# Kernel tuning notes

Measured on AMD Instinct MI355X. Metric: run time of the kernel, lower is better.

## Reference

```python
import jax, jax.numpy as jnp
import numpy as np


def setup_inputs() -> dict:
    key = jax.random.key(0)
    k1, k2 = jax.random.split(key)
    vortex_feature = jax.random.normal(k1, (2, 512, 6), dtype=jnp.float32)
    points = jax.random.normal(k2, (2, 256, 256, 2), dtype=jnp.float32)
    return {"vortex_feature": vortex_feature, "points": points}


def reference(vortex_feature, points):
    # vortex_feature: [B, N, 6] -> (y, x, tau, sig, v, u)
    y, x, tau, sig, v, u = [vortex_feature[..., i] for i in range(6)]
    loc = jnp.stack([y, x], axis=-1)            # [B, N, 2]

    # Broadcast: points [B, H, W, 1, 2] vs particle locations [B, 1, 1, N, 2]
    distances = points[..., None, :] - loc[:, None, None, :, :]   # [B, H, W, N, 2]
    sq_distance = jnp.sum(distances ** 2, axis=-1, keepdims=True)  # [B, H, W, N, 1]

    src_sigma = sig[:, None, None, :, None]     # [B, 1, 1, N, 1]
    src_strength = tau[:, None, None, :, None]  # [B, 1, 1, N, 1]

    falloff = jnp.exp(-sq_distance / src_sigma ** 2) / jnp.sqrt(sq_distance)
    strength = src_strength * falloff           # [B, H, W, N, 1]

    d1 = distances[..., 0]
    d2 = distances[..., 1]
    velocity = strength * jnp.stack([d2, -d1], axis=-1)  # [B, H, W, N, 2]
    return jnp.sum(velocity, axis=-2)           # [B, H, W, 2]
```

## Files before the change

### kernel.cpp

```cpp
#include <hip/hip_runtime.h>

#ifndef M_LOG2E_F
#define M_LOG2E_F 1.4426950408889634f
#endif

#if defined(__has_builtin)
#  if __has_builtin(__builtin_amdgcn_exp2f)
#    define FAST_EXP2(x) __builtin_amdgcn_exp2f(x)
#  else
#    define FAST_EXP2(x) exp2f(x)
#  endif
#  if __has_builtin(__builtin_amdgcn_rsqf)
#    define FAST_RSQ(x) __builtin_amdgcn_rsqf(x)
#  else
#    define FAST_RSQ(x) rsqrtf(x)
#  endif
#else
#  define FAST_EXP2(x) exp2f(x)
#  define FAST_RSQ(x) rsqrtf(x)
#endif

__global__ __launch_bounds__(256)
void GaussianFalloffKernel_83434034692733_kernel(
    const float* __restrict__ vortex,
    const float* __restrict__ points,
    float* __restrict__ out)
{
    constexpr int NV = 512;
    constexpr int PTS_PER_BATCH = 256 * 256;
    constexpr int BLOCKS_PER_BATCH = PTS_PER_BATCH / 256;

    __shared__ float4 sv[NV];

    const int b  = blockIdx.x / BLOCKS_PER_BATCH;
    const int pt = (blockIdx.x % BLOCKS_PER_BATCH) * 256 + threadIdx.x;

    const float* __restrict__ vb = vortex + (size_t)b * NV * 6;
    for (int v = threadIdx.x; v < NV; v += 256) {
        const float y   = vb[v * 6 + 0];
        const float x   = vb[v * 6 + 1];
        const float tau = vb[v * 6 + 2];
        const float sig = vb[v * 6 + 3];
        const float k   = M_LOG2E_F / (sig * sig);
        sv[v] = make_float4(y, x, tau, k);
    }
    __syncthreads();

    const float2 p = ((const float2*)points)[(size_t)b * PTS_PER_BATCH + pt];

    float acc0 = 0.0f;
    float acc1 = 0.0f;

    #pragma unroll 8
    for (int v = 0; v < NV; ++v) {
        const float4 s = sv[v];
        const float dy = p.x - s.x;
        const float dx = p.y - s.y;
        const float r2 = fmaf(dy, dy, dx * dx);
        const float e  = FAST_EXP2(-r2 * s.w);
        const float ri = FAST_RSQ(r2);
        const float f  = s.z * e * ri;
        acc0 = fmaf(f,  dx, acc0);
        acc1 = fmaf(f, -dy, acc1);
    }

    ((float2*)out)[(size_t)b * PTS_PER_BATCH + pt] = make_float2(acc0, acc1);
}

extern "C" void kernel_launch(void* const* d_in, const int* in_sizes, int n_in,
                              void* d_out, int out_size, void* d_ws, size_t ws_size,
                              hipStream_t stream) {
    const float* vortex = (const float*)d_in[0];
    const float* points = (const float*)d_in[1];
    float* out = (float*)d_out;

    const int blocks = 2 * 256;
    GaussianFalloffKernel_83434034692733_kernel<<<blocks, 256, 0, stream>>>(
        vortex, points, out);
}
```

Before: 80.51 us.

## Split vortex loop across four wavefronts, two points per thread with packed math

Each block now handles 128 points instead of 256. Its four wavefronts each sum a quarter of the vortices, and the partial sums are combined through shared memory. Each thread processes two points with 2-wide vector types so the compiler can emit packed FP32 ops, and each shared-memory vortex load now serves two points. The grid doubles to 1024 blocks to fill the CUs better. In exchange it adds a reduction step, an extra barrier and more shared memory.

Result: faster. 73.32 us (-8.9%).

```diff
diff --git a/kernel.cpp b/kernel.cpp
--- a/kernel.cpp
+++ b/kernel.cpp
@@ -1,8 +1,6 @@
 #include <hip/hip_runtime.h>
 
-#ifndef M_LOG2E_F
-#define M_LOG2E_F 1.4426950408889634f
-#endif
+typedef float v2f __attribute__((ext_vector_type(2)));
 
 #if defined(__has_builtin)
 #  if __has_builtin(__builtin_amdgcn_exp2f)
@@ -20,51 +18,73 @@
 #  define FAST_RSQ(x) rsqrtf(x)
 #endif
 
-__global__ __launch_bounds__(256)
+__global__ __launch_bounds__(256, 4)
 void GaussianFalloffKernel_83434034692733_kernel(
     const float* __restrict__ vortex,
     const float* __restrict__ points,
     float* __restrict__ out)
 {
     constexpr int NV = 512;
-    constexpr int PTS_PER_BATCH = 256 * 256;
-    constexpr int BLOCKS_PER_BATCH = PTS_PER_BATCH / 256;
+    constexpr int NQ = 4;
+    constexpr int VQ = NV / NQ;
+    constexpr int PTS_PER_BLOCK = 128;
+    constexpr int BLOCKS_PER_BATCH = 65536 / PTS_PER_BLOCK;
 
     __shared__ float4 sv[NV];
+    __shared__ v2f    red[NQ][PTS_PER_BLOCK];
 
-    const int b  = blockIdx.x / BLOCKS_PER_BATCH;
-    const int pt = (blockIdx.x % BLOCKS_PER_BATCH) * 256 + threadIdx.x;
+    const int b    = blockIdx.x / BLOCKS_PER_BATCH;
+    const int base = (blockIdx.x % BLOCKS_PER_BATCH) * PTS_PER_BLOCK;
+
+    const int tid = threadIdx.x;
+    const int q   = tid >> 6;
+    const int h   = tid & 63;
 
     const float* __restrict__ vb = vortex + (size_t)b * NV * 6;
-    for (int v = threadIdx.x; v < NV; v += 256) {
-        const float y   = vb[v * 6 + 0];
-        const float x   = vb[v * 6 + 1];
-        const float tau = vb[v * 6 + 2];
-        const float sig = vb[v * 6 + 3];
-        const float k   = M_LOG2E_F / (sig * sig);
-        sv[v] = make_float4(y, x, tau, k);
+    for (int v = tid; v < NV; v += 256) {
+        const float y    = vb[v * 6 + 0];
+        const float x    = vb[v * 6 + 1];
+        const float tau  = vb[v * 6 + 2];
+        const float sig  = vb[v * 6 + 3];
+        const float negk = -1.4426950408889634f / (sig * sig);
+        sv[v] = make_float4(y, x, tau, negk);
     }
     __syncthreads();
 
-    const float2 p = ((const float2*)points)[(size_t)b * PTS_PER_BATCH + pt];
+    const float2* __restrict__ pp =
+        (const float2*)points + (size_t)b * 65536 + base;
+    const float2 pA = pp[h];
+    const float2 pB = pp[h + 64];
+    const v2f py = { pA.x, pB.x };
+    const v2f px = { pA.y, pB.y };
 
-    float acc0 = 0.0f;
-    float acc1 = 0.0f;
+    v2f acc0 = { 0.0f, 0.0f };
+    v2f acc1 = { 0.0f, 0.0f };
 
+    const float4* __restrict__ svq = sv + q * VQ;
     #pragma unroll 8
-    for (int v = 0; v < NV; ++v) {
-        const float4 s = sv[v];
-        const float dy = p.x - s.x;
-        const float dx = p.y - s.y;
-        const float r2 = fmaf(dy, dy, dx * dx);
-        const float e  = FAST_EXP2(-r2 * s.w);
-        const float ri = FAST_RSQ(r2);
-        const float f  = s.z * e * ri;
-        acc0 = fmaf(f,  dx, acc0);
-        acc1 = fmaf(f, -dy, acc1);
+    for (int v = 0; v < VQ; ++v) {
+        const float4 s = svq[v];
+        const v2f dy = py - s.x;
+        const v2f dx = px - s.y;
+        const v2f r2 = dy * dy + dx * dx;
+        const v2f t  = r2 * s.w;
+        v2f e, ri;
+        e.x  = FAST_EXP2(t.x);  e.y  = FAST_EXP2(t.y);
+        ri.x = FAST_RSQ(r2.x);  ri.y = FAST_RSQ(r2.y);
+        const v2f f = (e * ri) * s.z;
+        acc0 += f * dx;
+        acc1 -= f * dy;
     }
 
-    ((float2*)out)[(size_t)b * PTS_PER_BATCH + pt] = make_float2(acc0, acc1);
+    red[q][h]      = (v2f){ acc0.x, acc1.x };
+    red[q][h + 64] = (v2f){ acc0.y, acc1.y };
+    __syncthreads();
+
+    if (tid < PTS_PER_BLOCK) {
+        const v2f s0 = red[0][tid] + red[1][tid] + red[2][tid] + red[3][tid];
+        ((float2*)out)[(size_t)b * 65536 + base + tid] = make_float2(s0.x, s0.y);
+    }
 }
 
 extern "C" void kernel_launch(void* const* d_in, const int* in_sizes, int n_in,
@@ -74,7 +94,7 @@
     const float* points = (const float*)d_in[1];
     float* out = (float*)d_out;
 
-    const int blocks = 2 * 256;
+    const int blocks = 2 * (65536 / 128);
     GaussianFalloffKernel_83434034692733_kernel<<<blocks, 256, 0, stream>>>(
         vortex, points, out);
 }
```
